# Kernel optimization log

Measured on AMD Instinct MI355X. Metric: run time of the kernel, lower is better.

The kernel has to match this reference:

```python
import jax, jax.numpy as jnp
import numpy as np

B, C, N, M, K = 1, 64, 65536, 65536, 16
H, O = 64, 128  # mlp hidden, out_channels


def setup_inputs() -> dict:
    key = jax.random.key(0)
    ks = jax.random.split(key, 8)
    return {
        "x": jax.random.normal(ks[0], (B, C, N), dtype=jnp.float32),
        "pos": jax.random.normal(ks[1], (B, 3, N), dtype=jnp.float32),
        "support_points": jax.random.normal(ks[2], (B, 3, M), dtype=jnp.float32),
        "W1": jax.random.normal(ks[3], (H, C + 3), dtype=jnp.float32) * 0.05,
        "b1": jax.random.normal(ks[4], (H,), dtype=jnp.float32) * 0.05,
        "W2": jax.random.normal(ks[5], (O, H), dtype=jnp.float32) * 0.05,
        "b2": jax.random.normal(ks[6], (O,), dtype=jnp.float32) * 0.05,
        "indices": jax.random.randint(ks[7], (B, M, K), 0, N, dtype=jnp.int64),
    }


def _gather_points(t, indices):
    # t: [B, C, N], indices: [B, M, K] -> [B, C, M, K]
    b, c, n = t.shape
    m, k = indices.shape[1], indices.shape[2]
    idx = indices.reshape(b, 1, m * k)  # broadcasts over channel dim
    return jnp.take_along_axis(t, idx, axis=2).reshape(b, c, m, k)


def reference(x, pos, support_points, W1, b1, W2, b2, indices):
    # gather neighbor features and positions: [B, C, M, K], [B, 3, M, K]
    feats = _gather_points(x, indices)
    pts = _gather_points(pos, indices) - support_points[:, :, :, None]
    h = jnp.concatenate([feats, pts], axis=1)  # [B, C+3, M, K]
    # shared per-point MLP (1x1 Conv2d == channel contraction)
    h = jnp.einsum("oc,bcmk->bomk", W1, h) + b1[None, :, None, None]
    h = jax.nn.relu(h)
    h = jnp.einsum("oc,bcmk->bomk", W2, h) + b2[None, :, None, None]
    # max-pool over neighborhood K -> [B, O, M]
    return jnp.max(h, axis=3)
```

## Files before the change

kernel.cpp:

```cpp
#include <hip/hip_runtime.h>

#define NPTS 65536
#define MPTS 65536

typedef __attribute__((ext_vector_type(8))) short bf16x8;
typedef __attribute__((ext_vector_type(4))) float f32x4;

__device__ __forceinline__ float bflo(unsigned int u){ union{unsigned int i; float f;} v; v.i = u<<16; return v.f; }
__device__ __forceinline__ float bfhi(unsigned int u){ union{unsigned int i; float f;} v; v.i = u & 0xffff0000u; return v.f; }
__device__ __forceinline__ unsigned short f2bf(float f){
  union{float f; unsigned int i;} v; v.f=f;
  unsigned int r = v.i + 0x7fffu + ((v.i>>16)&1u);
  return (unsigned short)(r>>16);
}
__device__ __forceinline__ unsigned int pk2(float a, float b){
  return (unsigned int)f2bf(a) | ((unsigned int)f2bf(b) << 16);
}

#define MFMA32(a,b,c) __builtin_amdgcn_mfma_f32_16x16x32_bf16((a),(b),(c),0,0,0)

__global__ __launch_bounds__(256) void pack_u(
    const float* __restrict__ x,
    const float* __restrict__ pos,
    const float* __restrict__ W1,
    const float* __restrict__ b1,
    const float* __restrict__ W2,
    unsigned short* __restrict__ U,
    unsigned short* __restrict__ W2F) {
  const int t = threadIdx.x;
  if (blockIdx.x >= 1024) {
    const int gg = (blockIdx.x - 1024) * 256 + t;
    if (gg < 1024) {
      const int g = gg >> 6, lane = gg & 63;
      const int q = lane >> 4, lr = lane & 15;
      const int kt = g >> 3, ot = g & 7;
      #pragma unroll
      for (int j = 0; j < 8; ++j)
        W2F[gg*8 + j] = f2bf(W2[(ot*16 + lr)*64 + kt*32 + q*8 + j]);
    }
    return;
  }
  const int lane = t & 63, w = t >> 6, quad = lane >> 4, lr = lane & 15;
  const int n = blockIdx.x * 64 + w * 16 + lr;

  bf16x8 wa[2][4], wt[4];
  #pragma unroll
  for (int kt = 0; kt < 2; ++kt)
    #pragma unroll
    for (int nt = 0; nt < 4; ++nt) {
      const float* r = W1 + (size_t)(nt*16 + lr)*67 + kt*32 + quad*8;
      const float4 a = *(const float4*)r;
      const float4 b = *(const float4*)(r + 4);
      union { unsigned int d[4]; bf16x8 v; } mk;
      mk.d[0] = pk2(a.x, a.y); mk.d[1] = pk2(a.z, a.w);
      mk.d[2] = pk2(b.x, b.y); mk.d[3] = pk2(b.z, b.w);
      wa[kt][nt] = mk.v;
    }
  #pragma unroll
  for (int nt = 0; nt < 4; ++nt) {
    union { unsigned int d[4]; bf16x8 v; } mk;
    mk.d[0] = 0u; mk.d[1] = 0u; mk.d[2] = 0u; mk.d[3] = 0u;
    if (quad == 0) {
      const float* r = W1 + (size_t)(nt*16 + lr)*67 + 64;
      mk.d[0] = pk2(r[0], r[1]);
      mk.d[1] = (unsigned int)f2bf(r[2]);
    }
    wt[nt] = mk.v;
  }

  const f32x4 fz = {0.f, 0.f, 0.f, 0.f};
  f32x4 acc[4] = {fz, fz, fz, fz};
  #pragma unroll
  for (int kt = 0; kt < 2; ++kt) {
    const float* xc = x + (size_t)(kt*32 + quad*8) * NPTS + n;
    union { unsigned int d[4]; bf16x8 v; } mk;
    #pragma unroll
    for (int i = 0; i < 4; ++i)
      mk.d[i] = pk2(xc[(size_t)(2*i) * NPTS], xc[(size_t)(2*i + 1) * NPTS]);
    #pragma unroll
    for (int nt = 0; nt < 4; ++nt)
      acc[nt] = MFMA32(wa[kt][nt], mk.v, acc[nt]);
  }
  {
    union { unsigned int d[4]; bf16x8 v; } mk;
    mk.d[0] = pk2(pos[n], pos[NPTS + n]);
    mk.d[1] = (unsigned int)f2bf(pos[2*NPTS + n]);
    mk.d[2] = 0u; mk.d[3] = 0u;
    #pragma unroll
    for (int nt = 0; nt < 4; ++nt)
      acc[nt] = MFMA32(wt[nt], mk.v, acc[nt]);
  }
  #pragma unroll
  for (int nt = 0; nt < 4; ++nt) {
    const float4 bb = *(const float4*)(b1 + nt*16 + quad*4);
    uint2 d;
    d.x = pk2(acc[nt][0] + bb.x, acc[nt][1] + bb.y);
    d.y = pk2(acc[nt][2] + bb.z, acc[nt][3] + bb.w);
    *(uint2*)(U + (size_t)n * 64 + nt*16 + quad*4) = d;
  }
}

__global__ __launch_bounds__(256, 4) void pointnet_reg(
    const unsigned short* __restrict__ U,
    const float* __restrict__ sup,
    const float* __restrict__ W1,
    const unsigned short* __restrict__ W2F,
    const float* __restrict__ b2,
    const int* __restrict__ indices,
    float* __restrict__ out) {
  const int t = threadIdx.x;
  const int m0 = blockIdx.x * 16;
  const int lane = t & 63, w = t >> 6, quad = lane >> 4, lr = lane & 15;
  const int wbase = m0 + w*4;

  int idx[4];
  #pragma unroll
  for (int pt = 0; pt < 4; ++pt) idx[pt] = indices[(wbase + pt)*16 + lr];

  uint4 ur[4][2];
  #pragma unroll
  for (int pt = 0; pt < 4; ++pt)
    #pragma unroll
    for (int kt = 0; kt < 2; ++kt)
      ur[pt][kt] = *(const uint4*)(U + (size_t)idx[pt]*64 + kt*32 + quad*8);

  float s0[4], s1[4], s2[4];
  #pragma unroll
  for (int pt = 0; pt < 4; ++pt) {
    s0[pt] = sup[wbase + pt];
    s1[pt] = sup[MPTS + wbase + pt];
    s2[pt] = sup[2*MPTS + wbase + pt];
  }

  bf16x8 ah[4][2];
  #pragma unroll
  for (int kt = 0; kt < 2; ++kt) {
    float w1p[8][3];
    #pragma unroll
    for (int j = 0; j < 8; ++j) {
      const float* r = W1 + (size_t)(kt*32 + quad*8 + j)*67 + 64;
      w1p[j][0] = r[0]; w1p[j][1] = r[1]; w1p[j][2] = r[2];
    }
    #pragma unroll
    for (int pt = 0; pt < 4; ++pt) {
      const unsigned int uu[4] = {ur[pt][kt].x, ur[pt][kt].y, ur[pt][kt].z, ur[pt][kt].w};
      union { unsigned int d[4]; bf16x8 v; } mk;
      #pragma unroll
      for (int i = 0; i < 4; ++i) {
        const float vl = w1p[2*i][0]*s0[pt] + w1p[2*i][1]*s1[pt] + w1p[2*i][2]*s2[pt];
        const float vh = w1p[2*i+1][0]*s0[pt] + w1p[2*i+1][1]*s1[pt] + w1p[2*i+1][2]*s2[pt];
        const float hl = fmaxf(bflo(uu[i]) - vl, 0.f);
        const float hh = fmaxf(bfhi(uu[i]) - vh, 0.f);
        mk.d[i] = pk2(hl, hh);
      }
      ah[pt][kt] = mk.v;
    }
  }

  const f32x4 fz = {0.f, 0.f, 0.f, 0.f};
  #pragma unroll
  for (int ot = 0; ot < 8; ++ot) {
    const bf16x8 wb0 = ((const bf16x8*)W2F)[(0*8 + ot)*64 + lane];
    const bf16x8 wb1 = ((const bf16x8*)W2F)[(1*8 + ot)*64 + lane];
    f32x4 a2[4];
    #pragma unroll
    for (int pt = 0; pt < 4; ++pt) {
      a2[pt] = MFMA32(ah[pt][0], wb0, fz);
      a2[pt] = MFMA32(ah[pt][1], wb1, a2[pt]);
    }
    float vm[4];
    #pragma unroll
    for (int pt = 0; pt < 4; ++pt) {
      float v = fmaxf(fmaxf(a2[pt][0], a2[pt][1]), fmaxf(a2[pt][2], a2[pt][3]));
      v = fmaxf(v, __shfl_xor(v, 16));
      v = fmaxf(v, __shfl_xor(v, 32));
      vm[pt] = v;
    }
    const float vq = (quad & 1) ? ((quad & 2) ? vm[3] : vm[1])
                                : ((quad & 2) ? vm[2] : vm[0]);
    const int o = ot*16 + lr;
    out[(size_t)o * MPTS + wbase + quad] = vq + b2[o];
  }
}

__global__ __launch_bounds__(256) void pointnet_fallback(
    const float* __restrict__ x, const float* __restrict__ pos,
    const float* __restrict__ sup,
    const float* __restrict__ W1, const float* __restrict__ b1,
    const float* __restrict__ W2, const float* __restrict__ b2,
    const int* __restrict__ indices, float* __restrict__ out) {
  __shared__ float sfeat[16][68];
  __shared__ float shid[16][64];
  __shared__ float smax[4][128];
  __shared__ int sidx[16];
  const int t = threadIdx.x;
  const int m = blockIdx.x;
  if (t < 16) sidx[t] = indices[m*16 + t];
  const float sup0 = sup[m], sup1 = sup[MPTS + m], sup2 = sup[2*MPTS + m];
  __syncthreads();
  for (int u = t; u < 16*17; u += 256) {
    const int k = u / 17, c4 = (u - k*17) * 4;
    const int idx = sidx[k];
    float4 wv;
    if (c4 < 64) {
      wv.x = x[(size_t)(c4+0)*NPTS + idx]; wv.y = x[(size_t)(c4+1)*NPTS + idx];
      wv.z = x[(size_t)(c4+2)*NPTS + idx]; wv.w = x[(size_t)(c4+3)*NPTS + idx];
    } else {
      wv.x = pos[idx] - sup0; wv.y = pos[NPTS + idx] - sup1;
      wv.z = pos[2*NPTS + idx] - sup2; wv.w = 0.f;
    }
    *(float4*)&sfeat[k][c4] = wv;
  }
  const int h = t & 63, kg = t >> 6;
  float w1r[68];
  #pragma unroll
  for (int c = 0; c < 67; ++c) w1r[c] = W1[h*67 + c];
  w1r[67] = 0.f;
  const float bias1 = b1[h];
  __syncthreads();
  #pragma unroll
  for (int j = 0; j < 4; ++j) {
    const int k = kg*4 + j;
    float a = bias1;
    const float4* rr = (const float4*)sfeat[k];
    #pragma unroll
    for (int qq = 0; qq < 17; ++qq) {
      const float4 v = rr[qq];
      a += w1r[qq*4+0]*v.x + w1r[qq*4+1]*v.y + w1r[qq*4+2]*v.z + w1r[qq*4+3]*v.w;
    }
    shid[k][h] = fmaxf(a, 0.f);
  }
  const int ow = t & 63;
  float w2a[64], w2b[64];
  #pragma unroll
  for (int hh = 0; hh < 64; ++hh) { w2a[hh] = W2[ow*64 + hh]; w2b[hh] = W2[(ow+64)*64 + hh]; }
  __syncthreads();
  float mxa = -3.0e38f, mxb = -3.0e38f;
  #pragma unroll
  for (int j = 0; j < 4; ++j) {
    const int k = kg*4 + j;
    const float4* hr = (const float4*)shid[k];
    float pa = 0.f, pb = 0.f;
    #pragma unroll
    for (int qq = 0; qq < 16; ++qq) {
      const float4 v = hr[qq];
      pa += w2a[qq*4+0]*v.x + w2a[qq*4+1]*v.y + w2a[qq*4+2]*v.z + w2a[qq*4+3]*v.w;
      pb += w2b[qq*4+0]*v.x + w2b[qq*4+1]*v.y + w2b[qq*4+2]*v.z + w2b[qq*4+3]*v.w;
    }
    mxa = fmaxf(mxa, pa); mxb = fmaxf(mxb, pb);
  }
  smax[kg][ow] = mxa; smax[kg][64 + ow] = mxb;
  __syncthreads();
  if (t < 128) {
    out[(size_t)t * MPTS + m] =
        fmaxf(fmaxf(smax[0][t], smax[1][t]), fmaxf(smax[2][t], smax[3][t])) + b2[t];
  }
}

extern "C" void kernel_launch(void* const* d_in, const int* in_sizes, int n_in,
                              void* d_out, int out_size, void* d_ws, size_t ws_size,
                              hipStream_t stream) {
  const float* x   = (const float*)d_in[0];
  const float* pos = (const float*)d_in[1];
  const float* sup = (const float*)d_in[2];
  const float* W1  = (const float*)d_in[3];
  const float* b1  = (const float*)d_in[4];
  const float* W2  = (const float*)d_in[5];
  const float* b2  = (const float*)d_in[6];
  const int* indices = (const int*)d_in[7];
  float* out = (float*)d_out;

  const size_t U_BYTES   = (size_t)NPTS * 64 * 2;
  const size_t W2F_BYTES = 16 * 64 * 8 * 2;
  if (ws_size >= U_BYTES + W2F_BYTES) {
    unsigned short* U   = (unsigned short*)d_ws;
    unsigned short* W2F = (unsigned short*)((char*)d_ws + U_BYTES);
    pack_u<<<NPTS/64 + 4, 256, 0, stream>>>(x, pos, W1, b1, W2, U, W2F);
    pointnet_reg<<<MPTS/16, 256, 0, stream>>>(U, sup, W1, W2F, b2, indices, out);
  } else {
    pointnet_fallback<<<MPTS, 256, 0, stream>>>(x, pos, sup, W1, b1, W2, b2, indices, out);
  }
}
```

Baseline: 144.3 us.

## Process eight support points per wave and use packed bf16 conversion intrinsic

Result: faster. 136.0 us (-5.7%).

```diff
diff --git a/kernel.cpp b/kernel.cpp
--- a/kernel.cpp
+++ b/kernel.cpp
@@ -1,4 +1,5 @@
 #include <hip/hip_runtime.h>
+#include <hip/hip_bf16.h>
 
 #define NPTS 65536
 #define MPTS 65536
@@ -13,8 +14,11 @@
   unsigned int r = v.i + 0x7fffu + ((v.i>>16)&1u);
   return (unsigned short)(r>>16);
 }
-__device__ __forceinline__ unsigned int pk2(float a, float b){
-  return (unsigned int)f2bf(a) | ((unsigned int)f2bf(b) << 16);
+__device__ __forceinline__ unsigned int pk2f(float a, float b){
+  float2 tf; tf.x = a; tf.y = b;
+  union { __hip_bfloat162 h; unsigned int u; } c;
+  c.h = __float22bfloat162_rn(tf);
+  return c.u;
 }
 
 #define MFMA32(a,b,c) __builtin_amdgcn_mfma_f32_16x16x32_bf16((a),(b),(c),0,0,0)
@@ -35,8 +39,10 @@
       const int q = lane >> 4, lr = lane & 15;
       const int kt = g >> 3, ot = g & 7;
       #pragma unroll
-      for (int j = 0; j < 8; ++j)
-        W2F[gg*8 + j] = f2bf(W2[(ot*16 + lr)*64 + kt*32 + q*8 + j]);
+      for (int j = 0; j < 4; ++j)
+        *(unsigned int*)&W2F[gg*8 + 2*j] =
+            pk2f(W2[(ot*16 + lr)*64 + kt*32 + q*8 + 2*j],
+                 W2[(ot*16 + lr)*64 + kt*32 + q*8 + 2*j + 1]);
     }
     return;
   }
@@ -52,8 +58,8 @@
       const float4 a = *(const float4*)r;
       const float4 b = *(const float4*)(r + 4);
       union { unsigned int d[4]; bf16x8 v; } mk;
-      mk.d[0] = pk2(a.x, a.y); mk.d[1] = pk2(a.z, a.w);
-      mk.d[2] = pk2(b.x, b.y); mk.d[3] = pk2(b.z, b.w);
+      mk.d[0] = pk2f(a.x, a.y); mk.d[1] = pk2f(a.z, a.w);
+      mk.d[2] = pk2f(b.x, b.y); mk.d[3] = pk2f(b.z, b.w);
       wa[kt][nt] = mk.v;
     }
   #pragma unroll
@@ -62,7 +68,7 @@
     mk.d[0] = 0u; mk.d[1] = 0u; mk.d[2] = 0u; mk.d[3] = 0u;
     if (quad == 0) {
       const float* r = W1 + (size_t)(nt*16 + lr)*67 + 64;
-      mk.d[0] = pk2(r[0], r[1]);
+      mk.d[0] = pk2f(r[0], r[1]);
       mk.d[1] = (unsigned int)f2bf(r[2]);
     }
     wt[nt] = mk.v;
@@ -76,14 +82,14 @@
     union { unsigned int d[4]; bf16x8 v; } mk;
     #pragma unroll
     for (int i = 0; i < 4; ++i)
-      mk.d[i] = pk2(xc[(size_t)(2*i) * NPTS], xc[(size_t)(2*i + 1) * NPTS]);
+      mk.d[i] = pk2f(xc[(size_t)(2*i) * NPTS], xc[(size_t)(2*i + 1) * NPTS]);
     #pragma unroll
     for (int nt = 0; nt < 4; ++nt)
       acc[nt] = MFMA32(wa[kt][nt], mk.v, acc[nt]);
   }
   {
     union { unsigned int d[4]; bf16x8 v; } mk;
-    mk.d[0] = pk2(pos[n], pos[NPTS + n]);
+    mk.d[0] = pk2f(pos[n], pos[NPTS + n]);
     mk.d[1] = (unsigned int)f2bf(pos[2*NPTS + n]);
     mk.d[2] = 0u; mk.d[3] = 0u;
     #pragma unroll
@@ -94,13 +100,13 @@
   for (int nt = 0; nt < 4; ++nt) {
     const float4 bb = *(const float4*)(b1 + nt*16 + quad*4);
     uint2 d;
-    d.x = pk2(acc[nt][0] + bb.x, acc[nt][1] + bb.y);
-    d.y = pk2(acc[nt][2] + bb.z, acc[nt][3] + bb.w);
+    d.x = pk2f(acc[nt][0] + bb.x, acc[nt][1] + bb.y);
+    d.y = pk2f(acc[nt][2] + bb.z, acc[nt][3] + bb.w);
     *(uint2*)(U + (size_t)n * 64 + nt*16 + quad*4) = d;
   }
 }
 
-__global__ __launch_bounds__(256, 4) void pointnet_reg(
+__global__ __launch_bounds__(256, 3) void pointnet_reg(
     const unsigned short* __restrict__ U,
     const float* __restrict__ sup,
     const float* __restrict__ W1,
@@ -109,30 +115,21 @@
     const int* __restrict__ indices,
     float* __restrict__ out) {
   const int t = threadIdx.x;
-  const int m0 = blockIdx.x * 16;
   const int lane = t & 63, w = t >> 6, quad = lane >> 4, lr = lane & 15;
-  const int wbase = m0 + w*4;
-
-  int idx[4];
-  #pragma unroll
-  for (int pt = 0; pt < 4; ++pt) idx[pt] = indices[(wbase + pt)*16 + lr];
-
-  uint4 ur[4][2];
-  #pragma unroll
-  for (int pt = 0; pt < 4; ++pt)
+  const int wbase = blockIdx.x * 32 + w * 8;
+
+  int idx[8];
+  #pragma unroll
+  for (int pt = 0; pt < 8; ++pt) idx[pt] = indices[(wbase + pt)*16 + lr];
+
+  uint4 ur[8][2];
+  #pragma unroll
+  for (int pt = 0; pt < 8; ++pt)
     #pragma unroll
     for (int kt = 0; kt < 2; ++kt)
       ur[pt][kt] = *(const uint4*)(U + (size_t)idx[pt]*64 + kt*32 + quad*8);
 
-  float s0[4], s1[4], s2[4];
-  #pragma unroll
-  for (int pt = 0; pt < 4; ++pt) {
-    s0[pt] = sup[wbase + pt];
-    s1[pt] = sup[MPTS + wbase + pt];
-    s2[pt] = sup[2*MPTS + wbase + pt];
-  }
-
-  bf16x8 ah[4][2];
+  bf16x8 ah[8][2];
   #pragma unroll
   for (int kt = 0; kt < 2; ++kt) {
     float w1p[8][3];
@@ -142,16 +139,19 @@
       w1p[j][0] = r[0]; w1p[j][1] = r[1]; w1p[j][2] = r[2];
     }
     #pragma unroll
-    for (int pt = 0; pt < 4; ++pt) {
+    for (int pt = 0; pt < 8; ++pt) {
+      const float s0 = sup[wbase + pt];
+      const float s1 = sup[MPTS + wbase + pt];
+      const float s2 = sup[2*MPTS + wbase + pt];
       const unsigned int uu[4] = {ur[pt][kt].x, ur[pt][kt].y, ur[pt][kt].z, ur[pt][kt].w};
       union { unsigned int d[4]; bf16x8 v; } mk;
       #pragma unroll
       for (int i = 0; i < 4; ++i) {
-        const float vl = w1p[2*i][0]*s0[pt] + w1p[2*i][1]*s1[pt] + w1p[2*i][2]*s2[pt];
-        const float vh = w1p[2*i+1][0]*s0[pt] + w1p[2*i+1][1]*s1[pt] + w1p[2*i+1][2]*s2[pt];
+        const float vl = w1p[2*i][0]*s0 + w1p[2*i][1]*s1 + w1p[2*i][2]*s2;
+        const float vh = w1p[2*i+1][0]*s0 + w1p[2*i+1][1]*s1 + w1p[2*i+1][2]*s2;
         const float hl = fmaxf(bflo(uu[i]) - vl, 0.f);
         const float hh = fmaxf(bfhi(uu[i]) - vh, 0.f);
-        mk.d[i] = pk2(hl, hh);
+        mk.d[i] = pk2f(hl, hh);
       }
       ah[pt][kt] = mk.v;
     }
@@ -162,24 +162,24 @@
   for (int ot = 0; ot < 8; ++ot) {
     const bf16x8 wb0 = ((const bf16x8*)W2F)[(0*8 + ot)*64 + lane];
     const bf16x8 wb1 = ((const bf16x8*)W2F)[(1*8 + ot)*64 + lane];
-    f32x4 a2[4];
-    #pragma unroll
-    for (int pt = 0; pt < 4; ++pt) {
-      a2[pt] = MFMA32(ah[pt][0], wb0, fz);
-      a2[pt] = MFMA32(ah[pt][1], wb1, a2[pt]);
-    }
-    float vm[4];
-    #pragma unroll
-    for (int pt = 0; pt < 4; ++pt) {
-      float v = fmaxf(fmaxf(a2[pt][0], a2[pt][1]), fmaxf(a2[pt][2], a2[pt][3]));
+    float vm[8];
+    #pragma unroll
+    for (int pt = 0; pt < 8; ++pt) {
+      f32x4 a2 = MFMA32(ah[pt][0], wb0, fz);
+      a2 = MFMA32(ah[pt][1], wb1, a2);
+      float v = fmaxf(fmaxf(a2[0], a2[1]), fmaxf(a2[2], a2[3]));
       v = fmaxf(v, __shfl_xor(v, 16));
       v = fmaxf(v, __shfl_xor(v, 32));
       vm[pt] = v;
     }
-    const float vq = (quad & 1) ? ((quad & 2) ? vm[3] : vm[1])
+    const int o = ot*16 + lr;
+    const float bb = b2[o];
+    const float va = (quad & 1) ? ((quad & 2) ? vm[3] : vm[1])
                                 : ((quad & 2) ? vm[2] : vm[0]);
-    const int o = ot*16 + lr;
-    out[(size_t)o * MPTS + wbase + quad] = vq + b2[o];
+    const float vb = (quad & 1) ? ((quad & 2) ? vm[7] : vm[5])
+                                : ((quad & 2) ? vm[6] : vm[4]);
+    out[(size_t)o * MPTS + wbase + quad] = va + bb;
+    out[(size_t)o * MPTS + wbase + 4 + quad] = vb + bb;
   }
 }
 
@@ -276,7 +276,7 @@
     unsigned short* U   = (unsigned short*)d_ws;
     unsigned short* W2F = (unsigned short*)((char*)d_ws + U_BYTES);
     pack_u<<<NPTS/64 + 4, 256, 0, stream>>>(x, pos, W1, b1, W2, U, W2F);
-    pointnet_reg<<<MPTS/16, 256, 0, stream>>>(U, sup, W1, W2F, b2, indices, out);
+    pointnet_reg<<<MPTS/32, 256, 0, stream>>>(U, sup, W1, W2F, b2, indices, out);
   } else {
     pointnet_fallback<<<MPTS, 256, 0, stream>>>(x, pos, sup, W1, b1, W2, b2, indices, out);
   }
```
